# Kernel tuning notes

Measured on AMD Instinct MI355X. Metric: run time of the kernel, lower is better.

The kernel has to match this reference:

```python
import jax, jax.numpy as jnp
import numpy as np


def reference(x, phi, sigma, M_phi_plus, M_phi_minus, M_u, padded_sl):
    """STU forward: spectral FFT convolution + autoregressive input term.

    x:   (B, L, D) input sequence
    phi: (L, K) time-domain spectral filters (top-K Hankel eigenvectors);
         V = rfft(phi, n=padded_sl) matches the module's precomputed V.
    sigma: (K,) Hankel eigenvalues
    M_phi_plus/minus: (K, D, D) per-filter projections
    M_u: (k_u, D, D) AR-on-input matrices
    """
    B, L, D = x.shape
    K = sigma.shape[0]
    n = padded_sl  # FFT length for causal linear convolution

    # Alternating-sign trick for the 'minus' featurization:
    # sum_j (-1)^j phi_j u_{t-j} = (-1)^t * conv(phi, sgn*u)_t
    sgn = jnp.where(jnp.arange(L) % 2 == 0, 1.0, -1.0).astype(x.dtype)[None, :, None]  # (1,L,1)

    V = jnp.fft.rfft(phi, n=n, axis=0)                       # (n//2+1, K) complex
    U = jnp.fft.rfft(jnp.stack([x, x * sgn], axis=-1), n=n, axis=1)  # (B, n//2+1, D, 2)
    prod = V[None, :, :, None, None] * U[:, :, None, :, :]    # (B, n//2+1, K, D, 2)
    conv = jnp.fft.irfft(prod, n=n, axis=1)[:, :L]            # (B, L, K, D, 2) causal conv
    U_plus = conv[..., 0]
    U_minus = conv[..., 1] * sgn[..., None]                   # undo sign on output side

    # Fold sigma^{1/4} scaling into the projection matrices.
    sig4 = (sigma ** 0.25).astype(x.dtype)[:, None, None]     # (K,1,1)
    spectral = (
        jnp.einsum('blkd,kdo->blo', U_plus, M_phi_plus * sig4)
        + jnp.einsum('blkd,kdo->blo', U_minus, M_phi_minus * sig4)
    )

    # compute_ar_u: y_t += sum_{i=0}^{k_u-1} x_{t-i} @ M_u[i]  (use_ar_u=True)
    ar_u = jnp.einsum('bld,do->blo', x, M_u[0])
    for i in range(1, M_u.shape[0]):  # small fixed depth k_u=3
        x_shift = jnp.pad(x, ((0, 0), (i, 0), (0, 0)))[:, :L]
        ar_u = ar_u + jnp.einsum('bld,do->blo', x_shift, M_u[i])

    # use_ar_y=False branch; dropout=0 (identity)
    return spectral + ar_u


def setup_inputs() -> dict:
    key = jax.random.key(0)
    ks = jax.random.split(key, 6)
    B, L, D, K, KU, N = 1, 2048, 768, 16, 3, 4096
    x = jax.random.normal(ks[0], (B, L, D), jnp.float32)
    phi = jax.random.normal(ks[1], (L, K), jnp.float32) / np.sqrt(L).astype(np.float32)
    sigma = jax.random.uniform(ks[2], (K,), jnp.float32, 0.1, 1.0)
    M_phi_plus = jax.random.normal(ks[3], (K, D, D), jnp.float32) * 0.02
    M_phi_minus = jax.random.normal(ks[4], (K, D, D), jnp.float32) * 0.02
    M_u = jax.random.normal(ks[5], (KU, D, D), jnp.float32) * 0.02
    return {"x": x, "phi": phi, "sigma": sigma, "M_phi_plus": M_phi_plus,
            "M_phi_minus": M_phi_minus, "M_u": M_u, "padded_sl": N}
```

## Files before the change

kernel.cpp:

```cpp
#include <hip/hip_runtime.h>

typedef __attribute__((ext_vector_type(8))) short bf16x8;
typedef __attribute__((ext_vector_type(4))) float f32x4;

#define SL 2048
#define DM 768
#define NCH 32
#define MSPEC 24576
#define MTOT  26880

#define SPLITK 10
#define KSLICE 2688
#define NT2 42
#define NITER2 21

#define WS_U      0
#define WS_TMAT   110100480ULL
#define WS_XT     126910464ULL
#define WS_MCAT   130056192ULL
#define WS_PART   171343872ULL
#define WS_NEED   234258432ULL

__device__ __forceinline__ short f2bf(float f) {
  unsigned u = __builtin_bit_cast(unsigned, f);
  u = (u + 0x7FFFu + ((u >> 16) & 1u)) >> 16;
  return (short)u;
}

__device__ __forceinline__ void gload16(const short* g, short* l) {
  __builtin_amdgcn_global_load_lds(
      (const __attribute__((address_space(1))) void*)g,
      (__attribute__((address_space(3))) void*)l, 16, 0, 0);
}


__global__ __launch_bounds__(256) void k_zero(float4* out) {
  out[blockIdx.x * 256 + threadIdx.x] = float4{0.f, 0.f, 0.f, 0.f};
}

__global__ __launch_bounds__(256) void k_prep_xT(const float* __restrict__ x,
                                                 short* __restrict__ xT) {
  __shared__ short tile[64][65];
  const int d0 = blockIdx.x * 64, l0 = blockIdx.y * 64;
  const int t = threadIdx.x;
#pragma unroll
  for (int rr = 0; rr < 16; ++rr) {
    int ll = rr * 4 + (t >> 6), dl = t & 63;
    tile[ll][dl] = f2bf(x[(size_t)(l0 + ll) * DM + d0 + dl]);
  }
  __syncthreads();
#pragma unroll
  for (int rr = 0; rr < 16; ++rr) {
    int dl = rr * 4 + (t >> 6), ll = t & 63;
    xT[(size_t)(d0 + dl) * SL + l0 + ll] = tile[ll][dl];
  }
}

__global__ __launch_bounds__(256) void k_prep_ar(const float* __restrict__ x,
                                                 short* __restrict__ U) {
  int id = blockIdx.x * 256 + threadIdx.x;
  int l = id / DM, d = id - l * DM;
#pragma unroll
  for (int i = 0; i < 3; ++i) {
    short v = 0;
    if (l >= i) v = f2bf(x[(size_t)(l - i) * DM + d]);
    U[(size_t)l * MTOT + MSPEC + i * DM + d] = v;
  }
}

__global__ __launch_bounds__(256) void k_prep_T(const float* __restrict__ phi,
                                                short* __restrict__ Tmat) {
  int idx = blockIdx.x * 256 + threadIdx.x;
  int c = idx >> 18;
  if (c >= 32) { Tmat[idx] = 0; return; }
  int b = idx & 127, a = (idx >> 7) & 127, dlag = (idx >> 14) & 15;
  int j = dlag * 128 + a - b;
  short v = 0;
  if (j >= 0) {
    float p = phi[j * 16 + (c & 15)];
    if (c >= 16 && (j & 1)) p = -p;
    v = f2bf(p);
  }
  Tmat[idx] = v;
}

__global__ __launch_bounds__(256) void k_prep_M(const float* __restrict__ Mp,
                                                const float* __restrict__ Mm,
                                                const float* __restrict__ Mu,
                                                const float* __restrict__ sigma,
                                                short* __restrict__ McatT) {
  __shared__ short tile[64][65];
  const int m0 = blockIdx.x * 64, o0 = blockIdx.y * 64;
  const int t = threadIdx.x;
#pragma unroll
  for (int rr = 0; rr < 16; ++rr) {
    int ml = rr * 4 + (t >> 6), ol = t & 63;
    int m = m0 + ml, o = o0 + ol;
    float v;
    if (m < MSPEC) {
      int c = m / DM, d = m - c * DM;
      int k = c & 15;
      float s4 = sqrtf(sqrtf(sigma[k]));
      if (c < 16) v = Mp[((size_t)c * DM + d) * DM + o] * s4;
      else        v = Mm[((size_t)(c - 16) * DM + d) * DM + o] * s4;
    } else {
      int mm = m - MSPEC;
      int i = mm / DM, d = mm - i * DM;
      v = Mu[((size_t)i * DM + d) * DM + o];
    }
    tile[ml][ol] = f2bf(v);
  }
  __syncthreads();
#pragma unroll
  for (int rr = 0; rr < 16; ++rr) {
    int ol = rr * 4 + (t >> 6), ml = t & 63;
    McatT[(size_t)(o0 + ol) * MTOT + m0 + ml] = tile[ml][ol];
  }
}


#define LDSREADS(BUF, KS, MQ)                                                   \
    _Pragma("unroll")                                                           \
    for (int q_ = 0; q_ < 4; ++q_)                                              \
      af_[q_] = *reinterpret_cast<const bf16x8*>(                               \
          &As[BUF][KS][wm1][((MQ) * 64 + q_ * 16 + lrow) * 32 + foff]);         \
    if ((MQ) == 0) {                                                            \
      _Pragma("unroll")                                                         \
      for (int i_ = 0; i_ < 4; ++i_)                                            \
        bf_[i_] = *reinterpret_cast<const bf16x8*>(                             \
            &Bs[BUF][KS][hB][(rB0 + i_ * 16 + lrow) * 32 + foff]);              \
    }

#define DOMFMA(MQ)                                                              \
    _Pragma("unroll")                                                           \
    for (int q_ = 0; q_ < 4; ++q_)                                              \
      _Pragma("unroll")                                                         \
      for (int i_ = 0; i_ < 4; ++i_)                                            \
        acc[(MQ) * 4 + q_][i_] = __builtin_amdgcn_mfma_f32_16x16x32_bf16(       \
            af_[q_], bf_[i_], acc[(MQ) * 4 + q_][i_], 0, 0, 0)

#define PHASE(BUF, KS, MQ, VMODE, STG) do {                                     \
    asm volatile("" ::: "memory");            \
    bf16x8 af_[4];                                                              \
    if ((VMODE) == 1) asm volatile("s_waitcnt vmcnt(6)" ::: "memory");          \
    if ((VMODE) == 2) {                                                         \
      if (j < nIterM1) asm volatile("s_waitcnt vmcnt(6)" ::: "memory");         \
      else             asm volatile("s_waitcnt vmcnt(0)" ::: "memory");         \
    }                                                                           \
    if ((VMODE) == 0) { LDSREADS(BUF, KS, MQ) }                                 \
    STG;                                                                        \
    __builtin_amdgcn_s_barrier();                                               \
    asm volatile("" ::: "memory");                                              \
    if ((VMODE) != 0) { LDSREADS(BUF, KS, MQ) }                                 \
    asm volatile("s_waitcnt lgkmcnt(0)" ::: "memory");                          \
    __builtin_amdgcn_sched_barrier(0);                                          \
    __builtin_amdgcn_s_setprio(1);                                              \
    DOMFMA(MQ);                                                                 \
    __builtin_amdgcn_s_setprio(0);                                              \
    __builtin_amdgcn_s_barrier();                                               \
  } while (0)


#define STA1(SBUF, SKS, SKT) do { int kt_ = (SKT); if (kt_ < nT) {              \
    int kch_ = kt_ * 64 + (SKS) * 32;                                           \
    int kb_ = kch_ >> 7, bo_ = kch_ & 127;                                      \
    int dl_ = 2 * rt - kb_;                                                     \
    const short* g0_ = (dl_ >= 0) ? (Tc + ((size_t)dl_ << 14) + bo_)            \
                                  : (Tz + bo_);                                 \
    const short* g1_ = Tc + ((size_t)(dl_ + 1) << 14) + bo_;                    \
    gload16(g0_, &As[SBUF][SKS][0][t8]);                                        \
    gload16(g1_, &As[SBUF][SKS][1][t8]); } } while (0)

#define STB1(SBUF, SKS, SKT) do { int kt_ = (SKT); if (kt_ < nT) {              \
    const short* g_ = Bb + kt_ * 64 + (SKS) * 32;                               \
    gload16(g_, &Bs[SBUF][SKS][0][t8]);                                         \
    gload16(g_ + (size_t)128 * SL, &Bs[SBUF][SKS][1][t8]); } } while (0)

__global__ __launch_bounds__(512, 2) void k_gemm1_8p(const short* __restrict__ Tmat,
                                                     const short* __restrict__ xT,
                                                     short* __restrict__ U) {
  __shared__ __align__(16) short As[2][2][2][4096];
  __shared__ __align__(16) short Bs[2][2][2][4096];
  const int bid = blockIdx.x;
  const int xcd = bid & 7;
  const int slot = bid >> 3;
  const int c = xcd * 4 + (slot & 3);
  const int q = slot >> 2;
  const int ct = q % 3;
  const int rt = 7 - q / 3;
  const int nT = 4 * (rt + 1);
  const int nIter = 2 * (rt + 1);
  const int nIterM1 = nIter - 1;
  const int t = threadIdx.x;
  const int lane = t & 63, wave = t >> 6;
  const int wm1 = wave >> 2;
  const int hB = (wave & 3) >> 1;
  const int rB0 = (wave & 1) * 64;
  const int lrow = lane & 15, quad = lane >> 4;
  const int foff = (quad ^ ((lrow >> 1) & 3)) << 3;
  const int r = t >> 2;
  const int cswz = ((t & 3) ^ ((r >> 1) & 3)) << 3;
  const int t8 = t * 8;

  const short* Tc = Tmat + ((size_t)(c * 16) << 14) + r * 128 + cswz;
  const short* Tz = Tmat + ((size_t)512 << 14) + r * 128 + cswz;
  const short* Bb = xT + (size_t)(ct * 256 + r) * SL + cswz;

  f32x4 acc[8][4] = {};

  STB1(0, 0, 0); STA1(0, 0, 0); STB1(0, 1, 0); STA1(0, 1, 0);
  STB1(1, 0, 1); STA1(1, 0, 1); STB1(1, 1, 1);

  for (int j = 0; j < nIter; ++j) {
    bf16x8 bf_[4];
    PHASE(0, 0, 0, 1, STA1(1, 1, 2 * j + 1));
    PHASE(0, 0, 1, 0, STB1(0, 0, 2 * j + 2));
    PHASE(0, 1, 0, 0, STA1(0, 0, 2 * j + 2));
    PHASE(0, 1, 1, 0, STB1(0, 1, 2 * j + 2));
    PHASE(1, 0, 0, 2, STA1(0, 1, 2 * j + 2));
    PHASE(1, 0, 1, 0, STB1(1, 0, 2 * j + 3));
    PHASE(1, 1, 0, 0, STA1(1, 0, 2 * j + 3));
    PHASE(1, 1, 1, 0, STB1(1, 1, 2 * j + 3));
  }

  const int wm128 = (wave >> 2) * 128, wn64 = (wave & 3) * 64;
  const int l0 = rt * 256, colbase = c * DM + ct * 256;
#pragma unroll
  for (int im = 0; im < 8; ++im)
#pragma unroll
    for (int in = 0; in < 4; ++in)
#pragma unroll
      for (int r4 = 0; r4 < 4; ++r4) {
        int row = l0 + wm128 + im * 16 + quad * 4 + r4;
        int col = colbase + wn64 + in * 16 + lrow;
        U[(size_t)row * MTOT + col] = f2bf(acc[im][in][r4]);
      }
}


#define STA2(SBUF, SKS, SKT) do { int kt_ = (SKT); if (kt_ < NT2) {             \
    const short* g_ = Abase + kt_ * 64 + (SKS) * 32;                            \
    gload16(g_, &As[SBUF][SKS][0][t8]);                                         \
    gload16(g_ + (size_t)128 * MTOT, &As[SBUF][SKS][1][t8]); } } while (0)

#define STB2(SBUF, SKS, SKT) do { int kt_ = (SKT); if (kt_ < NT2) {             \
    const short* g_ = Bbase + kt_ * 64 + (SKS) * 32;                            \
    gload16(g_, &Bs[SBUF][SKS][0][t8]);                                         \
    gload16(g_ + (size_t)128 * MTOT, &Bs[SBUF][SKS][1][t8]); } } while (0)

__global__ __launch_bounds__(512, 2) void k_gemm2_8p(const short* __restrict__ U,
                                                     const short* __restrict__ McatT,
                                                     float* __restrict__ out,
                                                     float* __restrict__ part,
                                                     int use_part) {
  __shared__ __align__(16) short As[2][2][2][4096];
  __shared__ __align__(16) short Bs[2][2][2][4096];
  const int bid = blockIdx.x;
  const int tile = bid % 24, kc = bid / 24;
  const int mt = tile & 7, nt_ = tile >> 3;
  const int m0 = mt * 256, o0 = nt_ * 256;
  const int kbase = kc * KSLICE;
  const int t = threadIdx.x;
  const int lane = t & 63, wave = t >> 6;
  const int wm1 = wave >> 2;
  const int hB = (wave & 3) >> 1;
  const int rB0 = (wave & 1) * 64;
  const int lrow = lane & 15, quad = lane >> 4;
  const int foff = (quad ^ ((lrow >> 1) & 3)) << 3;
  const int r = t >> 2;
  const int cswz = ((t & 3) ^ ((r >> 1) & 3)) << 3;
  const int t8 = t * 8;
  const int nIterM1 = NITER2 - 1;

  const short* Abase = U     + (size_t)(m0 + r) * MTOT + kbase + cswz;
  const short* Bbase = McatT + (size_t)(o0 + r) * MTOT + kbase + cswz;

  f32x4 acc[8][4] = {};

  STB2(0, 0, 0); STA2(0, 0, 0); STB2(0, 1, 0); STA2(0, 1, 0);
  STB2(1, 0, 1); STA2(1, 0, 1); STB2(1, 1, 1);

  for (int j = 0; j < NITER2; ++j) {
    bf16x8 bf_[4];
    PHASE(0, 0, 0, 1, STA2(1, 1, 2 * j + 1));
    PHASE(0, 0, 1, 0, STB2(0, 0, 2 * j + 2));
    PHASE(0, 1, 0, 0, STA2(0, 0, 2 * j + 2));
    PHASE(0, 1, 1, 0, STB2(0, 1, 2 * j + 2));
    PHASE(1, 0, 0, 2, STA2(0, 1, 2 * j + 2));
    PHASE(1, 0, 1, 0, STB2(1, 0, 2 * j + 3));
    PHASE(1, 1, 0, 0, STA2(1, 0, 2 * j + 3));
    PHASE(1, 1, 1, 0, STB2(1, 1, 2 * j + 3));
  }

  const int wm128 = (wave >> 2) * 128, wn64 = (wave & 3) * 64;
  if (use_part) {
    float* dst = part + (size_t)kc * (2048 * 768);
#pragma unroll
    for (int im = 0; im < 8; ++im)
#pragma unroll
      for (int in = 0; in < 4; ++in)
#pragma unroll
        for (int r4 = 0; r4 < 4; ++r4) {
          int row = m0 + wm128 + im * 16 + quad * 4 + r4;
          int col = o0 + wn64 + in * 16 + lrow;
          dst[(size_t)row * DM + col] = acc[im][in][r4];
        }
  } else {
#pragma unroll
    for (int im = 0; im < 8; ++im)
#pragma unroll
      for (int in = 0; in < 4; ++in)
#pragma unroll
        for (int r4 = 0; r4 < 4; ++r4) {
          int row = m0 + wm128 + im * 16 + quad * 4 + r4;
          int col = o0 + wn64 + in * 16 + lrow;
          atomicAdd(&out[(size_t)row * DM + col], acc[im][in][r4]);
        }
  }
}

__global__ __launch_bounds__(256) void k_reduce(const float4* __restrict__ part,
                                                float4* __restrict__ out) {
  int i = blockIdx.x * 256 + threadIdx.x;
  float4 s = part[i];
#pragma unroll
  for (int k = 1; k < SPLITK; ++k) {
    float4 v = part[(size_t)k * 393216 + i];
    s.x += v.x; s.y += v.y; s.z += v.z; s.w += v.w;
  }
  out[i] = s;
}

extern "C" void kernel_launch(void* const* d_in, const int* in_sizes, int n_in,
                              void* d_out, int out_size, void* d_ws, size_t ws_size,
                              hipStream_t stream) {
  (void)in_sizes; (void)n_in; (void)out_size;
  const float* x     = (const float*)d_in[0];
  const float* phi   = (const float*)d_in[1];
  const float* sigma = (const float*)d_in[2];
  const float* Mp    = (const float*)d_in[3];
  const float* Mm    = (const float*)d_in[4];
  const float* Mu    = (const float*)d_in[5];
  float* out = (float*)d_out;
  char* ws = (char*)d_ws;

  short* U     = (short*)(ws + WS_U);
  short* Tmat  = (short*)(ws + WS_TMAT);
  short* xT    = (short*)(ws + WS_XT);
  short* McatT = (short*)(ws + WS_MCAT);
  float* Wpart = (float*)(ws + WS_PART);
  const int use_part = ws_size >= WS_NEED ? 1 : 0;

  if (!use_part)
    k_zero<<<dim3(1536), dim3(256), 0, stream>>>((float4*)out);
  k_prep_xT<<<dim3(12, 32), dim3(256), 0, stream>>>(x, xT);
  k_prep_ar<<<dim3(6144), dim3(256), 0, stream>>>(x, U);
  k_prep_T<<<dim3(32832), dim3(256), 0, stream>>>(phi, Tmat);
  k_prep_M<<<dim3(420, 12), dim3(256), 0, stream>>>(Mp, Mm, Mu, sigma, McatT);
  k_gemm1_8p<<<dim3(768), dim3(512), 0, stream>>>(Tmat, xT, U);
  k_gemm2_8p<<<dim3(240), dim3(512), 0, stream>>>(U, McatT, out, Wpart, use_part);
  if (use_part)
    k_reduce<<<dim3(1536), dim3(256), 0, stream>>>((const float4*)Wpart, (float4*)out);
}
```

Baseline: 386.0 us.

## Merge prep kernels into one launch, vectorize stores, reorder GEMM phase barriers

The four preprocessing kernels (M transpose/scale, Toeplitz T build, AR shift, x transpose) are fused into a single kernel that dispatches on block index, which removes three launches and the gaps between them. The T and AR builders now write 8 bf16 values per thread with vector stores. Separately, the GEMM PHASE macro drops the barrier and lgkmcnt wait before the MFMAs in the VMODE==0 path and moves the LDS wait to the end, so LDS reads can overlap with MFMA issue. The reordering risks MFMAs consuming LDS fragments before their reads complete if the compiler does not insert the needed waits.

```diff
diff --git a/kernel.cpp b/kernel.cpp
--- a/kernel.cpp
+++ b/kernel.cpp
@@ -1,6 +1,7 @@
 #include <hip/hip_runtime.h>
 
 typedef __attribute__((ext_vector_type(8))) short bf16x8;
+typedef __attribute__((ext_vector_type(8))) short short8;
 typedef __attribute__((ext_vector_type(4))) float f32x4;
 
 #define SL 2048
@@ -21,6 +22,12 @@
 #define WS_PART   171343872ULL
 #define WS_NEED   234258432ULL
 
+#define NB_M   5040
+#define NB_T   4104
+#define NB_AR  768
+#define NB_XT  384
+#define NB_ALL (NB_M + NB_T + NB_AR + NB_XT)
+
 __device__ __forceinline__ short f2bf(float f) {
   unsigned u = __builtin_bit_cast(unsigned, f);
   u = (u + 0x7FFFu + ((u >> 16) & 1u)) >> 16;
@@ -38,83 +45,97 @@
   out[blockIdx.x * 256 + threadIdx.x] = float4{0.f, 0.f, 0.f, 0.f};
 }
 
-__global__ __launch_bounds__(256) void k_prep_xT(const float* __restrict__ x,
-                                                 short* __restrict__ xT) {
+__global__ __launch_bounds__(256) void k_prep_all(const float* __restrict__ x,
+                                                  const float* __restrict__ phi,
+                                                  const float* __restrict__ sigma,
+                                                  const float* __restrict__ Mp,
+                                                  const float* __restrict__ Mm,
+                                                  const float* __restrict__ Mu,
+                                                  short* __restrict__ xT,
+                                                  short* __restrict__ U,
+                                                  short* __restrict__ Tmat,
+                                                  short* __restrict__ McatT) {
   __shared__ short tile[64][65];
-  const int d0 = blockIdx.x * 64, l0 = blockIdx.y * 64;
+  const int b = blockIdx.x;
   const int t = threadIdx.x;
-#pragma unroll
-  for (int rr = 0; rr < 16; ++rr) {
-    int ll = rr * 4 + (t >> 6), dl = t & 63;
-    tile[ll][dl] = f2bf(x[(size_t)(l0 + ll) * DM + d0 + dl]);
-  }
-  __syncthreads();
-#pragma unroll
-  for (int rr = 0; rr < 16; ++rr) {
-    int dl = rr * 4 + (t >> 6), ll = t & 63;
-    xT[(size_t)(d0 + dl) * SL + l0 + ll] = tile[ll][dl];
-  }
-}
-
-__global__ __launch_bounds__(256) void k_prep_ar(const float* __restrict__ x,
-                                                 short* __restrict__ U) {
-  int id = blockIdx.x * 256 + threadIdx.x;
-  int l = id / DM, d = id - l * DM;
-#pragma unroll
-  for (int i = 0; i < 3; ++i) {
-    short v = 0;
-    if (l >= i) v = f2bf(x[(size_t)(l - i) * DM + d]);
-    U[(size_t)l * MTOT + MSPEC + i * DM + d] = v;
-  }
-}
-
-__global__ __launch_bounds__(256) void k_prep_T(const float* __restrict__ phi,
-                                                short* __restrict__ Tmat) {
-  int idx = blockIdx.x * 256 + threadIdx.x;
-  int c = idx >> 18;
-  if (c >= 32) { Tmat[idx] = 0; return; }
-  int b = idx & 127, a = (idx >> 7) & 127, dlag = (idx >> 14) & 15;
-  int j = dlag * 128 + a - b;
-  short v = 0;
-  if (j >= 0) {
-    float p = phi[j * 16 + (c & 15)];
-    if (c >= 16 && (j & 1)) p = -p;
-    v = f2bf(p);
-  }
-  Tmat[idx] = v;
-}
-
-__global__ __launch_bounds__(256) void k_prep_M(const float* __restrict__ Mp,
-                                                const float* __restrict__ Mm,
-                                                const float* __restrict__ Mu,
-                                                const float* __restrict__ sigma,
-                                                short* __restrict__ McatT) {
-  __shared__ short tile[64][65];
-  const int m0 = blockIdx.x * 64, o0 = blockIdx.y * 64;
-  const int t = threadIdx.x;
-#pragma unroll
-  for (int rr = 0; rr < 16; ++rr) {
-    int ml = rr * 4 + (t >> 6), ol = t & 63;
-    int m = m0 + ml, o = o0 + ol;
-    float v;
-    if (m < MSPEC) {
-      int c = m / DM, d = m - c * DM;
-      int k = c & 15;
-      float s4 = sqrtf(sqrtf(sigma[k]));
-      if (c < 16) v = Mp[((size_t)c * DM + d) * DM + o] * s4;
-      else        v = Mm[((size_t)(c - 16) * DM + d) * DM + o] * s4;
-    } else {
-      int mm = m - MSPEC;
-      int i = mm / DM, d = mm - i * DM;
-      v = Mu[((size_t)i * DM + d) * DM + o];
-    }
-    tile[ml][ol] = f2bf(v);
-  }
-  __syncthreads();
-#pragma unroll
-  for (int rr = 0; rr < 16; ++rr) {
-    int ol = rr * 4 + (t >> 6), ml = t & 63;
-    McatT[(size_t)(o0 + ol) * MTOT + m0 + ml] = tile[ml][ol];
+
+  if (b < NB_M) {
+    const int m0 = (b % 420) * 64, o0 = (b / 420) * 64;
+#pragma unroll
+    for (int rr = 0; rr < 16; ++rr) {
+      int ml = rr * 4 + (t >> 6), ol = t & 63;
+      int m = m0 + ml, o = o0 + ol;
+      float v;
+      if (m < MSPEC) {
+        int c = m / DM, d = m - c * DM;
+        int k = c & 15;
+        float s4 = sqrtf(sqrtf(sigma[k]));
+        if (c < 16) v = Mp[((size_t)c * DM + d) * DM + o] * s4;
+        else        v = Mm[((size_t)(c - 16) * DM + d) * DM + o] * s4;
+      } else {
+        int mm = m - MSPEC;
+        int i = mm / DM, d = mm - i * DM;
+        v = Mu[((size_t)i * DM + d) * DM + o];
+      }
+      tile[ml][ol] = f2bf(v);
+    }
+    __syncthreads();
+#pragma unroll
+    for (int rr = 0; rr < 16; ++rr) {
+      int ol = rr * 4 + (t >> 6), ml = t & 63;
+      McatT[(size_t)(o0 + ol) * MTOT + m0 + ml] = tile[ml][ol];
+    }
+    return;
+  }
+  if (b < NB_M + NB_T) {
+    int idx = ((b - NB_M) * 256 + t) * 8;
+    int c = idx >> 18;
+    short8 v = {0, 0, 0, 0, 0, 0, 0, 0};
+    if (c < 32) {
+      int b0 = idx & 127, a = (idx >> 7) & 127, dlag = (idx >> 14) & 15;
+      int j0 = dlag * 128 + a - b0;
+#pragma unroll
+      for (int e = 0; e < 8; ++e) {
+        int j = j0 - e;
+        if (j >= 0) {
+          float p = phi[j * 16 + (c & 15)];
+          if (c >= 16 && (j & 1)) p = -p;
+          v[e] = f2bf(p);
+        }
+      }
+    }
+    *reinterpret_cast<short8*>(&Tmat[idx]) = v;
+    return;
+  }
+  if (b < NB_M + NB_T + NB_AR) {
+    int tid = (b - NB_M - NB_T) * 256 + t;
+    int l = tid / 96, d0 = (tid - l * 96) * 8;
+#pragma unroll
+    for (int i = 0; i < 3; ++i) {
+      short8 v = {0, 0, 0, 0, 0, 0, 0, 0};
+      if (l >= i) {
+        const float* src = &x[(size_t)(l - i) * DM + d0];
+#pragma unroll
+        for (int e = 0; e < 8; ++e) v[e] = f2bf(src[e]);
+      }
+      *reinterpret_cast<short8*>(&U[(size_t)l * MTOT + MSPEC + i * DM + d0]) = v;
+    }
+    return;
+  }
+  {
+    const int bb = b - NB_M - NB_T - NB_AR;
+    const int d0 = (bb % 12) * 64, l0 = (bb / 12) * 64;
+#pragma unroll
+    for (int rr = 0; rr < 16; ++rr) {
+      int ll = rr * 4 + (t >> 6), dl = t & 63;
+      tile[ll][dl] = f2bf(x[(size_t)(l0 + ll) * DM + d0 + dl]);
+    }
+    __syncthreads();
+#pragma unroll
+    for (int rr = 0; rr < 16; ++rr) {
+      int dl = rr * 4 + (t >> 6), ll = t & 63;
+      xT[(size_t)(d0 + dl) * SL + l0 + ll] = tile[ll][dl];
+    }
   }
 }
 
@@ -140,7 +161,6 @@
             af_[q_], bf_[i_], acc[(MQ) * 4 + q_][i_], 0, 0, 0)
 
 #define PHASE(BUF, KS, MQ, VMODE, STG) do {                                     \
-    asm volatile("" ::: "memory");            \
     bf16x8 af_[4];                                                              \
     if ((VMODE) == 1) asm volatile("s_waitcnt vmcnt(6)" ::: "memory");          \
     if ((VMODE) == 2) {                                                         \
@@ -149,14 +169,15 @@
     }                                                                           \
     if ((VMODE) == 0) { LDSREADS(BUF, KS, MQ) }                                 \
     STG;                                                                        \
-    __builtin_amdgcn_s_barrier();                                               \
-    asm volatile("" ::: "memory");                                              \
-    if ((VMODE) != 0) { LDSREADS(BUF, KS, MQ) }                                 \
-    asm volatile("s_waitcnt lgkmcnt(0)" ::: "memory");                          \
-    __builtin_amdgcn_sched_barrier(0);                                          \
+    if ((VMODE) != 0) {                                                         \
+      __builtin_amdgcn_s_barrier();                                             \
+      asm volatile("" ::: "memory");                                            \
+      LDSREADS(BUF, KS, MQ)                                                     \
+    }                                                                           \
     __builtin_amdgcn_s_setprio(1);                                              \
     DOMFMA(MQ);                                                                 \
     __builtin_amdgcn_s_setprio(0);                                              \
+    asm volatile("s_waitcnt lgkmcnt(0)" ::: "memory");                          \
     __builtin_amdgcn_s_barrier();                                               \
   } while (0)
 
@@ -353,10 +374,8 @@
 
   if (!use_part)
     k_zero<<<dim3(1536), dim3(256), 0, stream>>>((float4*)out);
-  k_prep_xT<<<dim3(12, 32), dim3(256), 0, stream>>>(x, xT);
-  k_prep_ar<<<dim3(6144), dim3(256), 0, stream>>>(x, U);
-  k_prep_T<<<dim3(32832), dim3(256), 0, stream>>>(phi, Tmat);
-  k_prep_M<<<dim3(420, 12), dim3(256), 0, stream>>>(Mp, Mm, Mu, sigma, McatT);
+  k_prep_all<<<dim3(NB_ALL), dim3(256), 0, stream>>>(x, phi, sigma, Mp, Mm, Mu,
+                                                     xT, U, Tmat, McatT);
   k_gemm1_8p<<<dim3(768), dim3(512), 0, stream>>>(Tmat, xT, U);
   k_gemm2_8p<<<dim3(240), dim3(512), 0, stream>>>(U, McatT, out, Wpart, use_part);
   if (use_part)
```

After: 367.3 us. 1.05x faster.
